# Kernel optimization log

Measured on AMD Instinct MI355X. Metric: run time of the kernel, lower is better.

## Reference

```python
import jax, jax.numpy as jnp
import numpy as np

H = 2048
E = 8
K = 2
INTER = 2048
T = 2048


def setup_inputs() -> dict:
    key = jax.random.key(0)
    k1, k2, k3 = jax.random.split(key, 3)
    hidden_4d = jax.random.normal(k1, (1, 1, T, H), dtype=jnp.float32)
    # learned per-expert fused gate+up projection: [1, E, H, 2*inter]
    gate_up_proj = jax.random.normal(k2, (1, E, H, INTER * 2), dtype=jnp.float32) * 0.02
    # binary (expert, token) dispatch mask: on average K of E experts active per token
    sparsity = (jax.random.uniform(k3, (1, E, T, 1)) < (K / E)).astype(jnp.float32)
    return {"hidden_4d": hidden_4d, "gate_up_proj": gate_up_proj, "sparsity": sparsity}


def reference(hidden_4d, gate_up_proj, sparsity):
    # sparse_matmul semantics: per-expert GEMM of tokens against expert weight
    # blocks, with output blocks zeroed (skipped) where the sparsity mask is 0.
    # hidden_4d: [1, 1, T, H]; gate_up_proj: [1, E, H, F]; sparsity: [1, E, T, 1]
    # out[a, e, t, f] = mask[a, e, t] * sum_h hidden[a, 0, t, h] * W[a, e, h, f]
    out = jnp.einsum("abth,aehf->aetf", hidden_4d, gate_up_proj) * sparsity
    return out.sum()
```

## Files before the change

kernel.cpp:

```cpp
#include <hip/hip_runtime.h>

#define H_DIM 2048
#define E_DIM 8
#define T_DIM 2048
#define F_DIM 4096
#define ROWS (E_DIM * H_DIM)
#define ROWSUM_BLOCKS (ROWS / 4)
#define HBLOCKS (H_DIM / 256)
#define TCHUNK 512
#define TCHUNKS (T_DIM / TCHUNK)
#define MS_BLOCKS (HBLOCKS * TCHUNKS)

typedef float f32x4 __attribute__((ext_vector_type(4)));


__global__ __launch_bounds__(256) void fused_compute(
    const float* __restrict__ hidden,
    const float* __restrict__ W,
    const float* __restrict__ mask,
    float* __restrict__ ws) {
  float* Bsum = ws;
  float* Ap   = ws + ROWS;

  int bid = blockIdx.x;
  if (bid >= MS_BLOCKS) {
    int wave = ((bid - MS_BLOCKS) << 2) | (threadIdx.x >> 6);
    int lane = threadIdx.x & 63;
    const f32x4* row = (const f32x4*)(W + (size_t)wave * F_DIM);
    float s = 0.f;
    #pragma unroll
    for (int i = 0; i < 16; ++i) {
      f32x4 v = __builtin_nontemporal_load(row + lane + (i << 6));
      s += (v.x + v.y) + (v.z + v.w);
    }
    #pragma unroll
    for (int off = 32; off > 0; off >>= 1)
      s += __shfl_down(s, off, 64);
    if (lane == 0) Bsum[wave] = s;
  } else {
    int hb = bid & (HBLOCKS - 1);
    int tc = bid >> 3;
    int h  = (hb << 8) + threadIdx.x;
    int t0 = tc * TCHUNK;

    __shared__ float m_lds[E_DIM][TCHUNK];
    #pragma unroll
    for (int i = 0; i < (E_DIM * TCHUNK) / 256; ++i) {
      int idx = i * 256 + threadIdx.x;
      int e = idx / TCHUNK, tt = idx % TCHUNK;
      m_lds[e][tt] = mask[e * T_DIM + t0 + tt];
    }
    __syncthreads();

    float acc[E_DIM];
    #pragma unroll
    for (int e = 0; e < E_DIM; ++e) acc[e] = 0.f;
    #pragma unroll 4
    for (int t = 0; t < TCHUNK; ++t) {
      float hv = hidden[(size_t)(t0 + t) * H_DIM + h];
      #pragma unroll
      for (int e = 0; e < E_DIM; ++e)
        acc[e] += hv * m_lds[e][t];
    }
    #pragma unroll
    for (int e = 0; e < E_DIM; ++e)
      Ap[(size_t)tc * ROWS + e * H_DIM + h] = acc[e];
  }
}

__global__ __launch_bounds__(1024) void dot_kernel(const float* __restrict__ ws,
                                                   float* __restrict__ out) {
  const float* Bsum = ws;
  const float* Ap   = ws + ROWS;
  float s = 0.f;
  #pragma unroll
  for (int i0 = 0; i0 < ROWS; i0 += 1024) {
    int i = i0 + threadIdx.x;
    float a = (Ap[i] + Ap[ROWS + i]) + (Ap[2 * ROWS + i] + Ap[3 * ROWS + i]);
    s += a * Bsum[i];
  }
  #pragma unroll
  for (int off = 32; off > 0; off >>= 1)
    s += __shfl_down(s, off, 64);
  __shared__ float red[16];
  int wave = threadIdx.x >> 6;
  int lane = threadIdx.x & 63;
  if (lane == 0) red[wave] = s;
  __syncthreads();
  if (threadIdx.x == 0) {
    float r = 0.f;
    #pragma unroll
    for (int w = 0; w < 16; ++w) r += red[w];
    out[0] = r;
  }
}

extern "C" void kernel_launch(void* const* d_in, const int* in_sizes, int n_in,
                              void* d_out, int out_size, void* d_ws, size_t ws_size,
                              hipStream_t stream) {
  const float* hidden = (const float*)d_in[0];
  const float* W      = (const float*)d_in[1];
  const float* mask   = (const float*)d_in[2];
  float* out = (float*)d_out;
  float* ws  = (float*)d_ws;

  fused_compute<<<ROWSUM_BLOCKS + MS_BLOCKS, 256, 0, stream>>>(hidden, W, mask, ws);
  dot_kernel<<<1, 1024, 0, stream>>>(ws, out);
}
```

Baseline: 400.4 us.

## Fuse final dot reduction into main kernel via last-block atomic counter

Merges the separate single-block dot kernel into the main kernel. Each block increments a global counter, and the last block to finish does the final reduction. The A-side mask-weighted hidden sum now uses 8 blocks with float4 vectorised loads and stores instead of 32 scalar blocks. A memset is added to reset the counter each call, which adds a small launch in place of the removed kernel. Fewer blocks on the A path risks that path becoming the tail, although the row-sum over W dominates.

```diff
diff --git a/kernel.cpp b/kernel.cpp
--- a/kernel.cpp
+++ b/kernel.cpp
@@ -5,94 +5,102 @@
 #define T_DIM 2048
 #define F_DIM 4096
 #define ROWS (E_DIM * H_DIM)
-#define ROWSUM_BLOCKS (ROWS / 4)
-#define HBLOCKS (H_DIM / 256)
+#define A_BLOCKS 8
 #define TCHUNK 512
-#define TCHUNKS (T_DIM / TCHUNK)
-#define MS_BLOCKS (HBLOCKS * TCHUNKS)
+#define TCHUNKS 4
+#define RS_BLOCKS (ROWS / 4)
+#define TOTAL_BLOCKS (A_BLOCKS + RS_BLOCKS)
+#define CTR_OFF (ROWS + TCHUNKS * ROWS)
 
 typedef float f32x4 __attribute__((ext_vector_type(4)));
 
 
-__global__ __launch_bounds__(256) void fused_compute(
+__global__ __launch_bounds__(256) void fused_all(
     const float* __restrict__ hidden,
     const float* __restrict__ W,
     const float* __restrict__ mask,
-    float* __restrict__ ws) {
+    float* __restrict__ ws,
+    float* __restrict__ out) {
   float* Bsum = ws;
   float* Ap   = ws + ROWS;
+  int* counter = (int*)(ws + CTR_OFF);
+
+  __shared__ float m_lds[E_DIM][TCHUNK];
+  __shared__ float red[4];
+  __shared__ int is_last;
 
   int bid = blockIdx.x;
-  if (bid >= MS_BLOCKS) {
-    int wave = ((bid - MS_BLOCKS) << 2) | (threadIdx.x >> 6);
-    int lane = threadIdx.x & 63;
-    const f32x4* row = (const f32x4*)(W + (size_t)wave * F_DIM);
-    float s = 0.f;
-    #pragma unroll
-    for (int i = 0; i < 16; ++i) {
-      f32x4 v = __builtin_nontemporal_load(row + lane + (i << 6));
-      s += (v.x + v.y) + (v.z + v.w);
-    }
-    #pragma unroll
-    for (int off = 32; off > 0; off >>= 1)
-      s += __shfl_down(s, off, 64);
-    if (lane == 0) Bsum[wave] = s;
-  } else {
-    int hb = bid & (HBLOCKS - 1);
-    int tc = bid >> 3;
-    int h  = (hb << 8) + threadIdx.x;
+  int tid = threadIdx.x;
+
+  if (bid < A_BLOCKS) {
+    int hb = bid & 1;
+    int tc = bid >> 1;
     int t0 = tc * TCHUNK;
+    int h4 = hb * 1024 + tid * 4;
 
-    __shared__ float m_lds[E_DIM][TCHUNK];
     #pragma unroll
     for (int i = 0; i < (E_DIM * TCHUNK) / 256; ++i) {
-      int idx = i * 256 + threadIdx.x;
-      int e = idx / TCHUNK, tt = idx % TCHUNK;
+      int idx = i * 256 + tid;
+      int e = idx >> 9, tt = idx & 511;
       m_lds[e][tt] = mask[e * T_DIM + t0 + tt];
     }
     __syncthreads();
 
-    float acc[E_DIM];
+    f32x4 acc[E_DIM];
     #pragma unroll
-    for (int e = 0; e < E_DIM; ++e) acc[e] = 0.f;
-    #pragma unroll 4
+    for (int e = 0; e < E_DIM; ++e) acc[e] = (f32x4)0.f;
+    #pragma unroll 2
     for (int t = 0; t < TCHUNK; ++t) {
-      float hv = hidden[(size_t)(t0 + t) * H_DIM + h];
+      f32x4 hv = *(const f32x4*)(hidden + (size_t)(t0 + t) * H_DIM + h4);
       #pragma unroll
       for (int e = 0; e < E_DIM; ++e)
         acc[e] += hv * m_lds[e][t];
     }
     #pragma unroll
     for (int e = 0; e < E_DIM; ++e)
-      Ap[(size_t)tc * ROWS + e * H_DIM + h] = acc[e];
+      *(f32x4*)(Ap + (size_t)tc * ROWS + e * H_DIM + h4) = acc[e];
+  } else {
+    int row  = ((bid - A_BLOCKS) << 2) | (tid >> 6);
+    int lane = tid & 63;
+    const f32x4* rp = (const f32x4*)(W + (size_t)row * F_DIM);
+    float s = 0.f;
+    #pragma unroll
+    for (int i = 0; i < 16; ++i) {
+      f32x4 v = __builtin_nontemporal_load(rp + lane + (i << 6));
+      s += (v.x + v.y) + (v.z + v.w);
+    }
+    #pragma unroll
+    for (int off = 32; off > 0; off >>= 1)
+      s += __shfl_down(s, off, 64);
+    if (lane == 0) Bsum[row] = s;
   }
-}
 
-__global__ __launch_bounds__(1024) void dot_kernel(const float* __restrict__ ws,
-                                                   float* __restrict__ out) {
-  const float* Bsum = ws;
-  const float* Ap   = ws + ROWS;
+  __threadfence();
+  __syncthreads();
+  if (tid == 0) {
+    int prev = atomicAdd(counter, 1);
+    is_last = (prev == TOTAL_BLOCKS - 1) ? 1 : 0;
+  }
+  __syncthreads();
+  if (!is_last) return;
+  __threadfence();
+
+  const f32x4* B4 = (const f32x4*)Bsum;
+  const f32x4* A4 = (const f32x4*)Ap;
   float s = 0.f;
   #pragma unroll
-  for (int i0 = 0; i0 < ROWS; i0 += 1024) {
-    int i = i0 + threadIdx.x;
-    float a = (Ap[i] + Ap[ROWS + i]) + (Ap[2 * ROWS + i] + Ap[3 * ROWS + i]);
-    s += a * Bsum[i];
+  for (int i0 = 0; i0 < ROWS / 4; i0 += 256) {
+    int i = i0 + tid;
+    f32x4 a = (A4[i] + A4[4096 + i]) + (A4[8192 + i] + A4[12288 + i]);
+    f32x4 b = B4[i];
+    s += (a.x * b.x + a.y * b.y) + (a.z * b.z + a.w * b.w);
   }
   #pragma unroll
   for (int off = 32; off > 0; off >>= 1)
     s += __shfl_down(s, off, 64);
-  __shared__ float red[16];
-  int wave = threadIdx.x >> 6;
-  int lane = threadIdx.x & 63;
-  if (lane == 0) red[wave] = s;
+  if ((tid & 63) == 0) red[tid >> 6] = s;
   __syncthreads();
-  if (threadIdx.x == 0) {
-    float r = 0.f;
-    #pragma unroll
-    for (int w = 0; w < 16; ++w) r += red[w];
-    out[0] = r;
-  }
+  if (tid == 0) out[0] = (red[0] + red[1]) + (red[2] + red[3]);
 }
 
 extern "C" void kernel_launch(void* const* d_in, const int* in_sizes, int n_in,
@@ -104,6 +112,6 @@
   float* out = (float*)d_out;
   float* ws  = (float*)d_ws;
 
-  fused_compute<<<ROWSUM_BLOCKS + MS_BLOCKS, 256, 0, stream>>>(hidden, W, mask, ws);
-  dot_kernel<<<1, 1024, 0, stream>>>(ws, out);
+  hipMemsetAsync((char*)d_ws + (size_t)CTR_OFF * 4, 0, 4, stream);
+  fused_all<<<TOTAL_BLOCKS, 256, 0, stream>>>(hidden, W, mask, ws, out);
 }
```

Result: slower. 1.201 ms (+200.0%).
